# Optimization experiments

Measured on AMD Instinct MI355X. Metric: run time of the kernel, lower is better.

Reference implementation:

```python
import jax, jax.numpy as jnp
import numpy as np

HEADS = 4
SIZE = 3


def setup_inputs() -> dict:
    key = jax.random.key(0)
    ks = jax.random.split(key, 8)
    B, C, D, H, W = 2, 64, 24, 24, 24
    s = 1.0 / np.sqrt(C)
    x = jax.random.normal(ks[0], (B, C, D, H, W), jnp.float32)
    cemb = jax.random.normal(ks[1], (B, C), jnp.float32)
    Wq = jax.random.normal(ks[2], (C, C), jnp.float32) * s
    bq = jax.random.normal(ks[3], (C,), jnp.float32) * 0.01
    Wk = jax.random.normal(ks[4], (C, C), jnp.float32) * s
    bk = jax.random.normal(ks[5], (C,), jnp.float32) * 0.01
    Wv = jax.random.normal(ks[6], (C, C), jnp.float32) * s
    bv = jax.random.normal(ks[7], (C,), jnp.float32) * 0.01
    return {"x": x, "cemb": cemb, "Wq": Wq, "bq": bq, "Wk": Wk, "bk": bk, "Wv": Wv, "bv": bv}


def _unfold(t, size, heads):
    # t: (B, D, H, W, C) -> (B, D*H*W, heads, size^3, C//heads), zero padded borders
    B, D, H, W, C = t.shape
    pad = size // 2
    tp = jnp.pad(t, ((0, 0), (pad, pad), (pad, pad), (pad, pad), (0, 0)))
    # depth shift outermost, then height, then width (matches torch unfold order)
    patches = jnp.stack(
        [tp[:, i:i + D, j:j + H, l:l + W, :]
         for i in range(size) for j in range(size) for l in range(size)],
        axis=4)  # (B, D, H, W, ws, C)
    ws = size ** 3
    hd = C // heads
    return patches.reshape(B, D * H * W, ws, heads, hd).transpose(0, 1, 3, 2, 4)


def reference(x, cemb, Wq, bq, Wk, bk, Wv, bv):
    # x: (B, C, D, H, W); cemb unused by the original forward
    B, C, D, H, W = x.shape
    heads, size = HEADS, SIZE
    hd = C // heads
    xc = jnp.transpose(x, (0, 2, 3, 4, 1))  # (B, D, H, W, C)
    q = xc @ Wq.T + bq
    k = xc @ Wk.T + bk
    v = xc @ Wv.T + bv
    kw = _unfold(k, size, heads)  # (B, N, h, ws, hd)
    vw = _unfold(v, size, heads)
    qh = q.reshape(B, D * H * W, heads, 1, hd) * (hd ** -0.5)
    attn = jnp.einsum('bnhqd,bnhkd->bnhqk', qh, kw)  # (B, N, h, 1, ws)
    attn = jax.nn.softmax(attn, axis=-1)
    h = jnp.einsum('bnhqk,bnhkd->bnhqd', attn, vw).reshape(B, D, H, W, C)
    out = xc + h
    return jnp.transpose(out, (0, 4, 1, 2, 3))
```

## Files before the change

kernel.cpp:

```cpp
#include <hip/hip_runtime.h>

#define NV 13824
#define CCH 64
#define NB 2

__global__ __launch_bounds__(256) void qkv_kernel(
    const float* __restrict__ x,
    const float* __restrict__ Wq, const float* __restrict__ bq,
    const float* __restrict__ Wk, const float* __restrict__ bk,
    const float* __restrict__ Wv, const float* __restrict__ bv,
    float* __restrict__ qo, float* __restrict__ ko, float* __restrict__ vo)
{
    __shared__ float sWT[3 * 64 * 64];
    __shared__ float sB[3 * 64];

    const int t   = threadIdx.x;
    const int bid = blockIdx.x;
    const int lb  = (bid & 7) * 54 + (bid >> 3);

    {
        const int o  = t & 63;
        const int kk = t >> 6;
        const float* const Ws[3] = {Wq, Wk, Wv};
        #pragma unroll
        for (int m = 0; m < 3; ++m) {
            const float* wm = Ws[m] + o * 64 + kk * 16;
            float* dd = sWT + m * 4096 + o;
            #pragma unroll
            for (int k4 = 0; k4 < 4; ++k4) {
                const float4 wv4 = *(const float4*)(wm + k4 * 4);
                dd[(kk * 16 + k4 * 4 + 0) * 64] = wv4.x;
                dd[(kk * 16 + k4 * 4 + 1) * 64] = wv4.y;
                dd[(kk * 16 + k4 * 4 + 2) * 64] = wv4.z;
                dd[(kk * 16 + k4 * 4 + 3) * 64] = wv4.w;
            }
        }
        if (t < 64) {
            sB[t]       = bq[t] * 0.25f;
            sB[64 + t]  = bk[t];
            sB[128 + t] = bv[t];
        }
    }
    __syncthreads();

    const int n0 = lb * 64;
    const int b  = n0 / NV;
    const int nn = n0 - b * NV;
    const int r0 = (t & 15) * 4;
    const int c0 = (t >> 4) * 4;

    const float* xb = x + (size_t)b * CCH * NV + nn + r0;

    float4 acc[3][4];
    #pragma unroll
    for (int m = 0; m < 3; ++m)
        #pragma unroll
        for (int c = 0; c < 4; ++c)
            acc[m][c] = make_float4(0.f, 0.f, 0.f, 0.f);

    #pragma unroll 8
    for (int k = 0; k < 64; ++k) {
        const float4 a = *(const float4*)(xb + (size_t)k * NV);
        #pragma unroll
        for (int m = 0; m < 3; ++m) {
            const float4 bb = *(const float4*)(sWT + m * 4096 + k * 64 + c0);
#define QKV_C(CI, S) { acc[m][CI].x += a.x*(S); acc[m][CI].y += a.y*(S); \
                       acc[m][CI].z += a.z*(S); acc[m][CI].w += a.w*(S); }
            QKV_C(0, bb.x) QKV_C(1, bb.y) QKV_C(2, bb.z) QKV_C(3, bb.w)
#undef QKV_C
        }
    }

    float* const outs[3] = {qo, ko, vo};
    #pragma unroll
    for (int m = 0; m < 3; ++m) {
        const float4 bb = *(const float4*)(sB + m * 64 + c0);
        const float  sc = (m == 0) ? 0.25f : 1.0f;
        float* ob = outs[m] + (size_t)(n0 + r0) * 64 + c0;
#define QKV_ROW(RR, F) { \
        const float4 o4 = make_float4(acc[m][0].F * sc + bb.x, \
                                      acc[m][1].F * sc + bb.y, \
                                      acc[m][2].F * sc + bb.z, \
                                      acc[m][3].F * sc + bb.w); \
        *(float4*)(ob + (size_t)(RR) * 64) = o4; }
        QKV_ROW(0, x) QKV_ROW(1, y) QKV_ROW(2, z) QKV_ROW(3, w)
#undef QKV_ROW
    }
}

__global__ __launch_bounds__(256) void attn_kernel(
    const float* __restrict__ x,
    const float* __restrict__ qw,
    const float* __restrict__ kw,
    const float* __restrict__ vw,
    float* __restrict__ out)
{
    __shared__ float so[32][65];

    const int t    = threadIdx.x;
    const int bid  = blockIdx.x;
    const int lb   = (bid & 7) * 108 + (bid >> 3);
    const int half = t & 1;
    const int head = (t >> 1) & 3;
    const int vb   = t >> 3;
    const int n0g  = lb * 32;
    const int gr   = n0g + vb;
    const int b    = gr / NV;
    const int n    = gr - b * NV;
    const int d    = n / 576;
    const int rem  = n - d * 576;
    const int r    = rem / 24;
    const int w    = rem - r * 24;
    const int coff = head * 16 + half * 8;

    int   idx[27];
    float msk[27];
    #pragma unroll
    for (int i3 = 0; i3 < 3; ++i3)
    #pragma unroll
    for (int j3 = 0; j3 < 3; ++j3)
    #pragma unroll
    for (int l3 = 0; l3 < 3; ++l3) {
        const int dd = d + i3 - 1;
        const int rr = r + j3 - 1;
        const int ww = w + l3 - 1;
        const bool ok = ((unsigned)dd < 24u) & ((unsigned)rr < 24u) & ((unsigned)ww < 24u);
        const int jj = (i3 * 3 + j3) * 3 + l3;
        idx[jj] = ok ? ((dd * 24 + rr) * 24 + ww) : n;
        msk[jj] = ok ? 1.f : 0.f;
    }

    const float4* qp = (const float4*)(qw + (size_t)gr * 64 + coff);
    const float4 q0 = qp[0], q1 = qp[1];

    const float* kbase = kw + (size_t)b * NV * 64 + coff;

    float logit[27];
    #pragma unroll
    for (int j = 0; j < 27; ++j) {
        const float4* kp = (const float4*)(kbase + (size_t)idx[j] * 64);
        const float4 k0 = kp[0], k1 = kp[1];
        float a;
        a  = q0.x * k0.x + q0.y * k0.y + q0.z * k0.z + q0.w * k0.w;
        a += q1.x * k1.x + q1.y * k1.y + q1.z * k1.z + q1.w * k1.w;
        logit[j] = a * msk[j];
    }
    #pragma unroll
    for (int j = 0; j < 27; ++j)
        logit[j] += __shfl_xor(logit[j], 1, 64);

    float ssum = 0.f;
    #pragma unroll
    for (int j = 0; j < 27; ++j) {
        const float e = __expf(logit[j]);
        logit[j] = e;
        ssum += e;
    }
    const float inv = 1.f / ssum;

    float a0=0.f,a1=0.f,a2=0.f,a3=0.f,a4=0.f,a5=0.f,a6=0.f,a7=0.f;
    const float* vbase = vw + (size_t)b * NV * 64 + coff;
    #pragma unroll
    for (int j = 0; j < 27; ++j) {
        const float p = logit[j] * msk[j];
        const float4* vp = (const float4*)(vbase + (size_t)idx[j] * 64);
        const float4 v0 = vp[0], v1 = vp[1];
        a0 += p * v0.x; a1 += p * v0.y; a2 += p * v0.z; a3 += p * v0.w;
        a4 += p * v1.x; a5 += p * v1.y; a6 += p * v1.z; a7 += p * v1.w;
    }

    so[vb][coff + 0] = a0 * inv;  so[vb][coff + 1] = a1 * inv;
    so[vb][coff + 2] = a2 * inv;  so[vb][coff + 3] = a3 * inv;
    so[vb][coff + 4] = a4 * inv;  so[vb][coff + 5] = a5 * inv;
    so[vb][coff + 6] = a6 * inv;  so[vb][coff + 7] = a7 * inv;
    __syncthreads();

    const int vv = t & 31;
    const int cg = t >> 5;
    const int bs = n0g / NV;
    const int nb0 = n0g - bs * NV;
    const float* xb = x   + (size_t)bs * CCH * NV + nb0 + vv;
    float*       ob = out + (size_t)bs * CCH * NV + nb0 + vv;
    #pragma unroll
    for (int i = 0; i < 8; ++i) {
        const int c = cg * 8 + i;
        ob[(size_t)c * NV] = xb[(size_t)c * NV] + so[vv][c];
    }
}

extern "C" void kernel_launch(void* const* d_in, const int* in_sizes, int n_in,
                              void* d_out, int out_size, void* d_ws, size_t ws_size,
                              hipStream_t stream) {
    const float* x  = (const float*)d_in[0];
    const float* Wq = (const float*)d_in[2];
    const float* bq = (const float*)d_in[3];
    const float* Wk = (const float*)d_in[4];
    const float* bk = (const float*)d_in[5];
    const float* Wv = (const float*)d_in[6];
    const float* bv = (const float*)d_in[7];
    float* out = (float*)d_out;

    float* ws = (float*)d_ws;
    const size_t RC = (size_t)NB * NV * CCH;
    float* q = ws;
    float* k = ws + RC;
    float* v = ws + 2 * RC;

    const int nrows = NB * NV;

    qkv_kernel<<<nrows / 64, 256, 0, stream>>>(x, Wq, bq, Wk, bk, Wv, bv, q, k, v);
    attn_kernel<<<nrows / 32, 256, 0, stream>>>(x, q, k, v, out);
}
```

Before: 107.8 us.

## Restructure QKV projection to keep x column in registers and read weights wave-uniformly

The QKV kernel drops the 48KB shared-memory transpose of all three weight matrices. Each lane now holds one voxel's 64 input channels in registers, and each wave computes 4 output channels per matrix using wave-uniform (scalar-friendly) weight row loads. Results are staged through a small padded shared tile so they can be written out coalesced, and the grid becomes 4x larger, with each block covering 16 output channels of a 64-voxel tile. In exchange, x is reloaded 4 times across blocks, and the 64-float register array may raise register pressure.

```diff
diff --git a/kernel.cpp b/kernel.cpp
--- a/kernel.cpp
+++ b/kernel.cpp
@@ -11,80 +11,56 @@
     const float* __restrict__ Wv, const float* __restrict__ bv,
     float* __restrict__ qo, float* __restrict__ ko, float* __restrict__ vo)
 {
-    __shared__ float sWT[3 * 64 * 64];
-    __shared__ float sB[3 * 64];
+    __shared__ float sb[3][64][20];
 
-    const int t   = threadIdx.x;
-    const int bid = blockIdx.x;
-    const int lb  = (bid & 7) * 54 + (bid >> 3);
+    const int t    = threadIdx.x;
+    const int bid  = blockIdx.x;
+    const int lb   = (bid & 7) * 216 + (bid >> 3);
+    const int tile = lb >> 2;
+    const int cqg  = lb & 3;
+    const int wid  = t >> 6;
+    const int lane = t & 63;
 
-    {
-        const int o  = t & 63;
-        const int kk = t >> 6;
-        const float* const Ws[3] = {Wq, Wk, Wv};
+    const int gr0 = tile * 64;
+    const int b   = gr0 / NV;
+    const int nn  = gr0 - b * NV;
+    const int n   = nn + lane;
+    const int c0  = __builtin_amdgcn_readfirstlane(cqg * 16 + wid * 4);
+
+    const float* xb = x + (size_t)b * CCH * NV + n;
+
+    float xr[64];
+    #pragma unroll
+    for (int k = 0; k < 64; ++k) xr[k] = xb[(size_t)k * NV];
+
+    const float* const Ws[3] = {Wq, Wk, Wv};
+    const float* const bs[3] = {bq, bk, bv};
+
+    #pragma unroll
+    for (int m = 0; m < 3; ++m) {
+        const float sc = (m == 0) ? 0.25f : 1.0f;
         #pragma unroll
-        for (int m = 0; m < 3; ++m) {
-            const float* wm = Ws[m] + o * 64 + kk * 16;
-            float* dd = sWT + m * 4096 + o;
+        for (int j = 0; j < 4; ++j) {
+            const float* row = Ws[m] + (size_t)(c0 + j) * 64;
+            float a = bs[m][c0 + j];
             #pragma unroll
-            for (int k4 = 0; k4 < 4; ++k4) {
-                const float4 wv4 = *(const float4*)(wm + k4 * 4);
-                dd[(kk * 16 + k4 * 4 + 0) * 64] = wv4.x;
-                dd[(kk * 16 + k4 * 4 + 1) * 64] = wv4.y;
-                dd[(kk * 16 + k4 * 4 + 2) * 64] = wv4.z;
-                dd[(kk * 16 + k4 * 4 + 3) * 64] = wv4.w;
+            for (int k4 = 0; k4 < 16; ++k4) {
+                const float4 wv = *(const float4*)(row + k4 * 4);
+                a += xr[k4 * 4 + 0] * wv.x + xr[k4 * 4 + 1] * wv.y
+                   + xr[k4 * 4 + 2] * wv.z + xr[k4 * 4 + 3] * wv.w;
             }
-        }
-        if (t < 64) {
-            sB[t]       = bq[t] * 0.25f;
-            sB[64 + t]  = bk[t];
-            sB[128 + t] = bv[t];
+            sb[m][lane][wid * 4 + j] = a * sc;
         }
     }
     __syncthreads();
 
-    const int n0 = lb * 64;
-    const int b  = n0 / NV;
-    const int nn = n0 - b * NV;
-    const int r0 = (t & 15) * 4;
-    const int c0 = (t >> 4) * 4;
-
-    const float* xb = x + (size_t)b * CCH * NV + nn + r0;
-
-    float4 acc[3][4];
-    #pragma unroll
-    for (int m = 0; m < 3; ++m)
-        #pragma unroll
-        for (int c = 0; c < 4; ++c)
-            acc[m][c] = make_float4(0.f, 0.f, 0.f, 0.f);
-
-    #pragma unroll 8
-    for (int k = 0; k < 64; ++k) {
-        const float4 a = *(const float4*)(xb + (size_t)k * NV);
-        #pragma unroll
-        for (int m = 0; m < 3; ++m) {
-            const float4 bb = *(const float4*)(sWT + m * 4096 + k * 64 + c0);
-#define QKV_C(CI, S) { acc[m][CI].x += a.x*(S); acc[m][CI].y += a.y*(S); \
-                       acc[m][CI].z += a.z*(S); acc[m][CI].w += a.w*(S); }
-            QKV_C(0, bb.x) QKV_C(1, bb.y) QKV_C(2, bb.z) QKV_C(3, bb.w)
-#undef QKV_C
-        }
-    }
-
+    const int v = t >> 2;
+    const int i = t & 3;
     float* const outs[3] = {qo, ko, vo};
     #pragma unroll
     for (int m = 0; m < 3; ++m) {
-        const float4 bb = *(const float4*)(sB + m * 64 + c0);
-        const float  sc = (m == 0) ? 0.25f : 1.0f;
-        float* ob = outs[m] + (size_t)(n0 + r0) * 64 + c0;
-#define QKV_ROW(RR, F) { \
-        const float4 o4 = make_float4(acc[m][0].F * sc + bb.x, \
-                                      acc[m][1].F * sc + bb.y, \
-                                      acc[m][2].F * sc + bb.z, \
-                                      acc[m][3].F * sc + bb.w); \
-        *(float4*)(ob + (size_t)(RR) * 64) = o4; }
-        QKV_ROW(0, x) QKV_ROW(1, y) QKV_ROW(2, z) QKV_ROW(3, w)
-#undef QKV_ROW
+        const float4 o4 = *(const float4*)(&sb[m][v][i * 4]);
+        *(float4*)(outs[m] + (size_t)(gr0 + v) * 64 + cqg * 16 + i * 4) = o4;
     }
 }
 
@@ -208,6 +184,6 @@
 
     const int nrows = NB * NV;
 
-    qkv_kernel<<<nrows / 64, 256, 0, stream>>>(x, Wq, bq, Wk, bk, Wv, bv, q, k, v);
+    qkv_kernel<<<nrows / 16, 256, 0, stream>>>(x, Wq, bq, Wk, bk, Wv, bv, q, k, v);
     attn_kernel<<<nrows / 32, 256, 0, stream>>>(x, q, k, v, out);
 }
```

New measurement: 112.8 us. 1.05x slower.
